# Optimization experiments

Hardware: AMD Instinct MI355X
Metric: run time of the kernel (lower is better)

## Reference

```python
import jax, jax.numpy as jnp
import numpy as np

H = 768   # hidden (cell) size
P = 256   # projection size
I = 80    # input feature dim
L = 3     # model_num_layers
B, T = 256, 400


def setup_inputs() -> dict:
    key = jax.random.key(0)
    ks = jax.random.split(key, 16)
    s = 0.05
    inp = {"x": jax.random.normal(ks[0], (B, T, I), dtype=jnp.float32)}
    in_dims = [I, P, P]
    for l in range(L):
        inp[f"Wx{l}"] = jax.random.normal(ks[1 + 4 * l], (in_dims[l], 4 * H), dtype=jnp.float32) * s
        inp[f"Wh{l}"] = jax.random.normal(ks[2 + 4 * l], (P, 4 * H), dtype=jnp.float32) * s
        inp[f"b{l}"] = jnp.zeros((4 * H,), dtype=jnp.float32)
        inp[f"Wp{l}"] = jax.random.normal(ks[3 + 4 * l], (H, P), dtype=jnp.float32) * s
    inp["W"] = jax.random.normal(ks[13], (P, P), dtype=jnp.float32) * s
    inp["lb"] = jnp.zeros((P,), dtype=jnp.float32)
    return inp


def _lstmp_layer(x, Wx, Wh, b, Wp, c0, h0):
    # Precompute input contribution to gates: [B, T, 4H]
    xg = jnp.einsum("bti,ig->btg", x, Wx) + b

    def step(carry, xg_t):
        c, h = carry
        gates = xg_t + h @ Wh              # [B, 4H]
        i, f, g, o = jnp.split(gates, 4, axis=-1)
        i = jax.nn.sigmoid(i)
        f = jax.nn.sigmoid(f)
        g = jnp.tanh(g)
        o = jax.nn.sigmoid(o)
        c = f * c + i * g                  # [B, H]
        h = (o * jnp.tanh(c)) @ Wp         # [B, P] projected hidden
        return (c, h), h

    (c, h), hs = jax.lax.scan(step, (c0, h0), jnp.swapaxes(xg, 0, 1))
    return jnp.swapaxes(hs, 0, 1), c, h   # seq_out [B,T,P], final c, h


def reference(x, Wx0, Wh0, b0, Wp0, Wx1, Wh1, b1, Wp1, Wx2, Wh2, b2, Wp2, W, lb):
    batch = x.shape[0]
    c = jnp.zeros((batch, H), dtype=x.dtype)
    h = jnp.zeros((batch, P), dtype=x.dtype)
    seq = x
    params = [(Wx0, Wh0, b0, Wp0), (Wx1, Wh1, b1, Wp1), (Wx2, Wh2, b2, Wp2)]
    for (Wx, Wh, b, Wp) in params:
        seq, c, h = _lstmp_layer(seq, Wx, Wh, b, Wp, c, h)
    embeds_raw = jax.nn.relu(seq.mean(axis=1) @ W.T + lb)   # [B, P]
    norm = jnp.linalg.norm(embeds_raw, axis=1, keepdims=True)
    return embeds_raw / norm
```

## Files before the change

kernel.cpp:

```cpp
#include <hip/hip_runtime.h>
#include <cstdint>
#include <cstddef>


typedef __attribute__((ext_vector_type(8))) short bf16x8;
typedef __attribute__((ext_vector_type(4))) float f32x4;
typedef __attribute__((ext_vector_type(2))) int i32x2;

#define TT 400
#define NB 256
#define IIP 96
#define HH 768
#define PP 256
#define G4 3072
#define WGJ 48
#define SMEMB (131072 + 2048)

__device__ __forceinline__ short f2bf(float f) {
  unsigned u = __builtin_bit_cast(unsigned, f);
  unsigned r = u + 0x7FFFu + ((u >> 16) & 1u);
  return (short)(r >> 16);
}
__device__ __forceinline__ float sigf(float x) { return 1.0f / (1.0f + __expf(-x)); }
__device__ __forceinline__ float tanh_(float x) { return 1.0f - 2.0f / (__expf(2.0f * x) + 1.0f); }

__device__ __forceinline__ void ld_co(bf16x8* d, const void* p) {
  asm volatile("global_load_dwordx4 %0, %1, off sc0 sc1" : "=v"(*d) : "v"(p));
}
__device__ __forceinline__ void st_co_b64(void* p, i32x2 v) {
  asm volatile("global_store_dwordx2 %0, %1, off sc0 sc1" :: "v"(p), "v"(v) : "memory");
}
__device__ __forceinline__ void st_co_b32(void* p, int v) {
  asm volatile("global_store_dword %0, %1, off sc0 sc1" :: "v"(p), "v"(v) : "memory");
}
#define WAIT_TIE24(u) \
  asm volatile("s_waitcnt vmcnt(0)" \
    : "+v"(u[0]),"+v"(u[1]),"+v"(u[2]),"+v"(u[3]),"+v"(u[4]),"+v"(u[5]), \
      "+v"(u[6]),"+v"(u[7]),"+v"(u[8]),"+v"(u[9]),"+v"(u[10]),"+v"(u[11]), \
      "+v"(u[12]),"+v"(u[13]),"+v"(u[14]),"+v"(u[15]),"+v"(u[16]),"+v"(u[17]), \
      "+v"(u[18]),"+v"(u[19]),"+v"(u[20]),"+v"(u[21]),"+v"(u[22]),"+v"(u[23]))


__global__ void k_xb(const float* __restrict__ x, short* __restrict__ xb) {
  int idx = blockIdx.x * 256 + threadIdx.x;
  if (idx >= TT * NB * 80) return;
  int i = idx % 80, tb = idx / 80;
  int b = tb % NB, t = tb / NB;
  xb[(size_t)(t * NB + b) * IIP + i] = f2bf(x[(size_t)(b * TT + t) * 80 + i]);
}

__global__ void k_makeB(const float* __restrict__ Wx, const float* __restrict__ Wp,
                        const float* __restrict__ Wh, short* __restrict__ out,
                        int K, int KIN, int INDIM) {
  int np = blockIdx.x * 256 + threadIdx.x;
  int k = blockIdx.y;
  int j2 = np >> 6, wj = np & 63, ntg = wj >> 4, cc = wj & 15;
  int col = ntg * HH + j2 * 16 + cc;
  float v;
  if (k < KIN) {
    v = (k < INDIM) ? Wx[(size_t)k * G4 + col] : 0.0f;
  } else {
    float a = 0.f;
    int kr = k - KIN;
    for (int q = 0; q < PP; ++q)
      a = fmaf(Wp[(size_t)kr * PP + q], Wh[(size_t)q * G4 + col], a);
    v = a;
  }
  out[(size_t)np * K + k] = f2bf(v);
}

__global__ void k_wpT(const float* __restrict__ Wp, short* __restrict__ WpT) {
  int idx = blockIdx.x * 256 + threadIdx.x;
  if (idx >= PP * HH) return;
  int n = idx % PP, k = idx / PP;
  WpT[(size_t)n * HH + k] = f2bf(Wp[(size_t)k * PP + n]);
}

__global__ void k_whT(const float* __restrict__ Wh, short* __restrict__ WhT) {
  int idx = blockIdx.x * 256 + threadIdx.x;
  if (idx >= G4 * PP) return;
  int np = idx % G4, k = idx / G4;
  int j2 = np >> 6, wj = np & 63, ntg = wj >> 4, cc = wj & 15;
  int col = ntg * HH + j2 * 16 + cc;
  WhT[(size_t)np * PP + k] = f2bf(Wh[(size_t)k * G4 + col]);
}

__global__ void k_pb(const float* b0, const float* b1, const float* b2, float* pb) {
  int n = blockIdx.x * 256 + threadIdx.x;
  if (n >= 3 * G4) return;
  int l = n / G4, np = n % G4;
  int j2 = np >> 6, wj = np & 63, ntg = wj >> 4, cc = wj & 15;
  int col = ntg * HH + j2 * 16 + cc;
  pb[n] = (l == 0 ? b0 : (l == 1 ? b1 : b2))[col];
}

__global__ void k_wt(const float* __restrict__ W, float* __restrict__ Wt) {
  int idx = blockIdx.x * 256 + threadIdx.x;
  int q = idx >> 8, p = idx & 255;
  Wt[idx] = W[p * 256 + q];
}


__device__ __forceinline__ void bar_arrive(int* slots, int j, int tid, int& arr) {
  asm volatile("s_waitcnt vmcnt(0)" ::: "memory");
  __syncthreads();
  ++arr;
  if (tid == 0) st_co_b32(slots + j * 4, arr);
}
__device__ __forceinline__ void bar_wait(const int* slots, int lane, int wv, int arr) {
  if (wv == 0) {
    const int* p = slots + (lane < 48 ? lane : 47) * 4;
    for (;;) {
      int v;
      asm volatile("global_load_dword %0, %1, off sc0 sc1\n\ts_waitcnt vmcnt(0)"
                   : "=v"(v) : "v"(p) : "memory");
      if (__all(v >= arr)) break;
      __builtin_amdgcn_s_sleep(1);
    }
  }
  __syncthreads();
}


template <int K>
__device__ __forceinline__ void stageB(const short* __restrict__ Bw, char* BsC, int j, int tid) {
  const char* src = (const char*)(Bw + (size_t)j * 64 * K);
  constexpr int UPR = K / 8;
  constexpr int ITERS = 64 * UPR / 256;
  #pragma unroll
  for (int it = 0; it < ITERS; ++it) {
    int u = it * 256 + tid;
    int wj = u / UPR;
    int k0 = (u - wj * UPR) * 8;
    bf16x8 v = *(const bf16x8*)(src + (size_t)wj * (K * 2) + k0 * 2);
    int gi = ((k0 >> 3) ^ (wj >> 1)) & 3;
    *(bf16x8*)(BsC + ((k0 >> 5) << 12) + (wj << 6) + (gi << 4)) = v;
  }
}


template <int CIN, bool DOPROJ, bool DOSUM>
__device__ __forceinline__ void layer_run(
    const char* BsC, short* UtS,
    const short* __restrict__ inS, const int inStr,
    const short* __restrict__ WpT, short* __restrict__ projOut,
    const float* __restrict__ pbL,
    short* __restrict__ U, int* slots,
    float* creg, float* sreg, f32x4* accInit,
    const int g, const int j, const int tid, int& arr)
{
  const int lane = tid & 63, wv = tid >> 6;
  const int c0 = lane & 15, rg = lane >> 4;
  const int row0 = g * 64;

  float bias[4];
  int fbB[4];
  #pragma unroll
  for (int nt = 0; nt < 4; ++nt) {
    bias[nt] = pbL[j * 64 + nt * 16 + c0];
    fbB[nt] = ((nt * 16 + c0) << 6) | (((rg ^ (c0 >> 1)) & 3) << 4);
  }
  const short* wb = DOPROJ ? (WpT + (size_t)(j * 16 + c0) * HH + rg * 8) : nullptr;

  for (int t = 0; t < TT; ++t) {
    const int pw = t & 1, pr = pw ^ 1;
    const short* aX = inS + (size_t)t * NB * inStr + (size_t)(row0 + wv * 16 + c0) * inStr + rg * 8;
    const short* aU = U + (size_t)pr * NB * HH + (size_t)(row0 + wv * 16 + c0) * HH + rg * 8;

    f32x4 zz = {0.f, 0.f, 0.f, 0.f};
    f32x4 acc[4];
    #pragma unroll
    for (int nt = 0; nt < 4; ++nt) acc[nt] = (t == 0) ? accInit[nt] : zz;

    bf16x8 xf[CIN];
    #pragma unroll
    for (int c = 0; c < CIN; ++c) xf[c] = *(const bf16x8*)(aX + c * 32);
    #pragma unroll
    for (int c = 0; c < CIN; ++c)
      #pragma unroll
      for (int nt = 0; nt < 4; ++nt)
        acc[nt] = __builtin_amdgcn_mfma_f32_16x16x32_bf16(
            xf[c], *(const bf16x8*)(BsC + (c << 12) + fbB[nt]), acc[nt], 0, 0, 0);

    if (t > 0) {
      bar_wait(slots, lane, wv, arr);
      bf16x8 uf[24];
      #pragma unroll
      for (int c = 0; c < 24; ++c) ld_co(&uf[c], aU + c * 32);
      WAIT_TIE24(uf);
      #pragma unroll
      for (int c = 0; c < 24; ++c)
        #pragma unroll
        for (int nt = 0; nt < 4; ++nt)
          acc[nt] = __builtin_amdgcn_mfma_f32_16x16x32_bf16(
              uf[c], *(const bf16x8*)(BsC + ((CIN + c) << 12) + fbB[nt]), acc[nt], 0, 0, 0);
      if (DOPROJ && j < 16) {
        f32x4 pacc = zz;
        #pragma unroll
        for (int c = 0; c < 24; ++c)
          pacc = __builtin_amdgcn_mfma_f32_16x16x32_bf16(
              uf[c], *(const bf16x8*)(wb + c * 32), pacc, 0, 0, 0);
        #pragma unroll
        for (int r = 0; r < 4; ++r)
          projOut[(size_t)(t - 1) * NB * PP + (size_t)(row0 + wv * 16 + rg * 4 + r) * PP + j * 16 + c0] = f2bf(pacc[r]);
      }
    }

    #pragma unroll
    for (int r = 0; r < 4; ++r) {
      float gi = acc[0][r] + bias[0];
      float gf = acc[1][r] + bias[1];
      float gg = acc[2][r] + bias[2];
      float go = acc[3][r] + bias[3];
      float cc2 = sigf(gf) * creg[r] + sigf(gi) * tanh_(gg);
      creg[r] = cc2;
      float uu = sigf(go) * tanh_(cc2);
      if (DOSUM) sreg[r] += uu;
      UtS[(wv * 16 + rg * 4 + r) * 16 + c0] = f2bf(uu);
    }
    __syncthreads();
    {
      int row = tid >> 2, q = tid & 3;
      i32x2 v = *(const i32x2*)(UtS + row * 16 + q * 4);
      st_co_b64((short*)U + (size_t)pw * NB * HH + (size_t)(row0 + row) * HH + j * 16 + q * 4, v);
    }
    bar_arrive(slots, j, tid, arr);
  }
}


__global__ void __launch_bounds__(256, 1) lstm_fused(
    const short* __restrict__ xb,
    const short* __restrict__ B0w, const short* __restrict__ B1w, const short* __restrict__ B2w,
    const float* __restrict__ pb,
    const short* __restrict__ WpT0, const short* __restrict__ WpT1,
    const short* __restrict__ WhT1, const short* __restrict__ WhT2,
    short* __restrict__ U, short* __restrict__ seqH,
    float* __restrict__ S, int* __restrict__ cnts)
{
  extern __shared__ char smem[];
  char* BsC = smem;
  short* UtS = (short*)(smem + 131072);
  const int bx = blockIdx.x;
  const int xcd = bx & 7;
  const int g = xcd >> 1;
  const int j = (xcd & 1) * 24 + (bx >> 3);
  const int tid = threadIdx.x;
  const int lane = tid & 63, wv = tid >> 6, c0 = lane & 15, rg = lane >> 4;
  const int row0 = g * 64;
  int* slots = cnts + g * 192;
  int arr = 0;
  float creg[4] = {0.f, 0.f, 0.f, 0.f}, sreg[4] = {0.f, 0.f, 0.f, 0.f};
  f32x4 zz = {0.f, 0.f, 0.f, 0.f};
  f32x4 accInit[4];
  #pragma unroll
  for (int nt = 0; nt < 4; ++nt) accInit[nt] = zz;

  stageB<864>(B0w, BsC, j, tid);
  __syncthreads();

  layer_run<3, true, false>(BsC, UtS, xb, IIP, WpT0, seqH, pb, U, slots,
                            creg, sreg, accInit, g, j, tid, arr);

  bar_wait(slots, lane, wv, arr);
  if (j < 16) {
    bf16x8 uf[24];
    const short* aU1 = U + (size_t)1 * NB * HH + (size_t)(row0 + wv * 16 + c0) * HH + rg * 8;
    #pragma unroll
    for (int c = 0; c < 24; ++c) ld_co(&uf[c], aU1 + c * 32);
    WAIT_TIE24(uf);
    const short* wb0 = WpT0 + (size_t)(j * 16 + c0) * HH + rg * 8;
    f32x4 pacc = zz;
    #pragma unroll
    for (int c = 0; c < 24; ++c)
      pacc = __builtin_amdgcn_mfma_f32_16x16x32_bf16(uf[c], *(const bf16x8*)(wb0 + c * 32), pacc, 0, 0, 0);
    #pragma unroll
    for (int r = 0; r < 4; ++r)
      seqH[(size_t)399 * NB * PP + (size_t)(row0 + wv * 16 + rg * 4 + r) * PP + j * 16 + c0] = f2bf(pacc[r]);
  }
  __threadfence();
  bar_arrive(slots, j, tid, arr);
  bar_wait(slots, lane, wv, arr);
  __threadfence();
  {
    const short* aseq = seqH + (size_t)399 * NB * PP + (size_t)(row0 + wv * 16 + c0) * PP + rg * 8;
    #pragma unroll
    for (int nt = 0; nt < 4; ++nt) accInit[nt] = zz;
    #pragma unroll
    for (int c = 0; c < 8; ++c) {
      bf16x8 a = *(const bf16x8*)(aseq + c * 32);
      #pragma unroll
      for (int nt = 0; nt < 4; ++nt) {
        bf16x8 b = *(const bf16x8*)(WhT1 + (size_t)(j * 64 + nt * 16 + c0) * PP + c * 32 + rg * 8);
        accInit[nt] = __builtin_amdgcn_mfma_f32_16x16x32_bf16(a, b, accInit[nt], 0, 0, 0);
      }
    }
  }
  __syncthreads();
  stageB<1024>(B1w, BsC, j, tid);
  __syncthreads();

  layer_run<8, true, false>(BsC, UtS, seqH, PP, WpT1, seqH, pb + G4, U, slots,
                            creg, sreg, accInit, g, j, tid, arr);

  bar_wait(slots, lane, wv, arr);
  if (j < 16) {
    bf16x8 uf[24];
    const short* aU1 = U + (size_t)1 * NB * HH + (size_t)(row0 + wv * 16 + c0) * HH + rg * 8;
    #pragma unroll
    for (int c = 0; c < 24; ++c) ld_co(&uf[c], aU1 + c * 32);
    WAIT_TIE24(uf);
    const short* wb1 = WpT1 + (size_t)(j * 16 + c0) * HH + rg * 8;
    f32x4 pacc = zz;
    #pragma unroll
    for (int c = 0; c < 24; ++c)
      pacc = __builtin_amdgcn_mfma_f32_16x16x32_bf16(uf[c], *(const bf16x8*)(wb1 + c * 32), pacc, 0, 0, 0);
    #pragma unroll
    for (int r = 0; r < 4; ++r)
      seqH[(size_t)399 * NB * PP + (size_t)(row0 + wv * 16 + rg * 4 + r) * PP + j * 16 + c0] = f2bf(pacc[r]);
  }
  __threadfence();
  bar_arrive(slots, j, tid, arr);
  bar_wait(slots, lane, wv, arr);
  __threadfence();
  {
    const short* aseq = seqH + (size_t)399 * NB * PP + (size_t)(row0 + wv * 16 + c0) * PP + rg * 8;
    #pragma unroll
    for (int nt = 0; nt < 4; ++nt) accInit[nt] = zz;
    #pragma unroll
    for (int c = 0; c < 8; ++c) {
      bf16x8 a = *(const bf16x8*)(aseq + c * 32);
      #pragma unroll
      for (int nt = 0; nt < 4; ++nt) {
        bf16x8 b = *(const bf16x8*)(WhT2 + (size_t)(j * 64 + nt * 16 + c0) * PP + c * 32 + rg * 8);
        accInit[nt] = __builtin_amdgcn_mfma_f32_16x16x32_bf16(a, b, accInit[nt], 0, 0, 0);
      }
    }
  }
  __syncthreads();
  stageB<1024>(B2w, BsC, j, tid);
  __syncthreads();

  layer_run<8, false, true>(BsC, UtS, seqH, PP, nullptr, nullptr, pb + 2 * G4, U, slots,
                            creg, sreg, accInit, g, j, tid, arr);

  #pragma unroll
  for (int r = 0; r < 4; ++r)
    S[(size_t)(row0 + wv * 16 + rg * 4 + r) * HH + j * 16 + c0] = sreg[r];
}


__global__ void k_mh(const float* __restrict__ S, const float* __restrict__ Wp2, float* __restrict__ mh) {
  __shared__ float sl[HH];
  int b = blockIdx.x, p = threadIdx.x;
  for (int i = p; i < HH; i += 256) sl[i] = S[(size_t)b * HH + i] * (1.0f / 400.0f);
  __syncthreads();
  float a = 0.f;
  for (int k = 0; k < HH; ++k) a = fmaf(sl[k], Wp2[(size_t)k * PP + p], a);
  mh[b * PP + p] = a;
}

__global__ void k_out(const float* __restrict__ mh, const float* __restrict__ Wt,
                      const float* __restrict__ lb, float* __restrict__ out) {
  __shared__ float ml[PP];
  __shared__ float red[PP];
  int b = blockIdx.x, p = threadIdx.x;
  ml[p] = mh[b * PP + p];
  __syncthreads();
  float z = lb[p];
  for (int q = 0; q < PP; ++q) z = fmaf(ml[q], Wt[q * PP + p], z);
  z = fmaxf(z, 0.0f);
  red[p] = z * z;
  __syncthreads();
  for (int st = 128; st > 0; st >>= 1) { if (p < st) red[p] += red[p + st]; __syncthreads(); }
  out[b * PP + p] = z / sqrtf(red[0]);
}


extern "C" void kernel_launch(void* const* d_in, const int* in_sizes, int n_in,
                              void* d_out, int out_size, void* d_ws, size_t ws_size,
                              hipStream_t stream) {
  (void)in_sizes; (void)n_in; (void)out_size; (void)ws_size;
  const float* x   = (const float*)d_in[0];
  const float* Wx0 = (const float*)d_in[1];
  const float* Wh0 = (const float*)d_in[2];
  const float* b0  = (const float*)d_in[3];
  const float* Wp0 = (const float*)d_in[4];
  const float* Wx1 = (const float*)d_in[5];
  const float* Wh1 = (const float*)d_in[6];
  const float* b1  = (const float*)d_in[7];
  const float* Wp1 = (const float*)d_in[8];
  const float* Wx2 = (const float*)d_in[9];
  const float* Wh2 = (const float*)d_in[10];
  const float* b2  = (const float*)d_in[11];
  const float* Wp2 = (const float*)d_in[12];
  const float* W   = (const float*)d_in[13];
  const float* lb  = (const float*)d_in[14];

  char* w = (char*)d_ws;
  auto take = [&](size_t bytes) { char* p = w; w += (bytes + 255) & ~(size_t)255; return p; };
  short* xb    = (short*)take((size_t)TT * NB * IIP * 2);
  short* B0w   = (short*)take((size_t)G4 * 864 * 2);
  short* B1w   = (short*)take((size_t)G4 * 1024 * 2);
  short* B2w   = (short*)take((size_t)G4 * 1024 * 2);
  float* pbw   = (float*)take((size_t)3 * G4 * 4);
  short* WpT0  = (short*)take((size_t)PP * HH * 2);
  short* WpT1  = (short*)take((size_t)PP * HH * 2);
  short* WhT1  = (short*)take((size_t)G4 * PP * 2);
  short* WhT2  = (short*)take((size_t)G4 * PP * 2);
  short* U     = (short*)take((size_t)2 * NB * HH * 2);
  short* seqH  = (short*)take((size_t)TT * NB * PP * 2);
  float* Sw    = (float*)take((size_t)NB * HH * 4);
  float* mhw   = (float*)take((size_t)NB * PP * 4);
  float* Wtw   = (float*)take((size_t)PP * PP * 4);
  int*   cnts  = (int*)take(4 * 192 * 4);

  hipMemsetAsync(xb, 0, (size_t)TT * NB * IIP * 2, stream);
  hipMemsetAsync(cnts, 0, 4 * 192 * 4, stream);

  k_xb<<<(TT * NB * 80 + 255) / 256, 256, 0, stream>>>(x, xb);
  k_makeB<<<dim3(12, 864), 256, 0, stream>>>(Wx0, Wp0, Wh0, B0w, 864, 96, 80);
  k_makeB<<<dim3(12, 1024), 256, 0, stream>>>(Wx1, Wp1, Wh1, B1w, 1024, 256, 256);
  k_makeB<<<dim3(12, 1024), 256, 0, stream>>>(Wx2, Wp2, Wh2, B2w, 1024, 256, 256);
  k_wpT<<<(PP * HH + 255) / 256, 256, 0, stream>>>(Wp0, WpT0);
  k_wpT<<<(PP * HH + 255) / 256, 256, 0, stream>>>(Wp1, WpT1);
  k_whT<<<(G4 * PP + 255) / 256, 256, 0, stream>>>(Wh1, WhT1);
  k_whT<<<(G4 * PP + 255) / 256, 256, 0, stream>>>(Wh2, WhT2);
  k_pb<<<(3 * G4 + 255) / 256, 256, 0, stream>>>(b0, b1, b2, pbw);
  k_wt<<<(PP * PP) / 256, 256, 0, stream>>>(W, Wtw);

  hipFuncSetAttribute((const void*)lstm_fused,
                      hipFuncAttributeMaxDynamicSharedMemorySize, SMEMB);
  lstm_fused<<<4 * WGJ, 256, SMEMB, stream>>>(xb, B0w, B1w, B2w, pbw, WpT0, WpT1,
                                              WhT1, WhT2, U, seqH, Sw, cnts);

  k_mh<<<NB, 256, 0, stream>>>(Sw, Wp2, mhw);
  k_out<<<NB, 256, 0, stream>>>(mhw, Wtw, lb, (float*)d_out);
}
```

Before: 11.95 ms.

## Split fused persistent LSTM into per-layer kernels with atomic-counter barriers

Replaces the single persistent kernel covering all three layers with one launch per layer, plus a small kernel that computes the initial hidden-to-gate term between layers. The per-workgroup flag-slot barrier becomes a single atomic counter per batch group that waits on a target count. The 24-load coherent asm block with its tied waitcnt becomes plain loads, and the projection MFMA is moved after the barrier arrive so it overlaps with other workgroups' progress. Projection stores now go through LDS and are written as coalesced 64-bit stores. This adds kernel launch overhead and a global round trip for the cell state and initial gates, and the plain (non-sc) loads of U may read stale cached data after the acquire fence.

```diff
diff --git a/kernel.cpp b/kernel.cpp
--- a/kernel.cpp
+++ b/kernel.cpp
@@ -24,21 +24,15 @@
 __device__ __forceinline__ float sigf(float x) { return 1.0f / (1.0f + __expf(-x)); }
 __device__ __forceinline__ float tanh_(float x) { return 1.0f - 2.0f / (__expf(2.0f * x) + 1.0f); }
 
-__device__ __forceinline__ void ld_co(bf16x8* d, const void* p) {
-  asm volatile("global_load_dwordx4 %0, %1, off sc0 sc1" : "=v"(*d) : "v"(p));
-}
 __device__ __forceinline__ void st_co_b64(void* p, i32x2 v) {
   asm volatile("global_store_dwordx2 %0, %1, off sc0 sc1" :: "v"(p), "v"(v) : "memory");
 }
-__device__ __forceinline__ void st_co_b32(void* p, int v) {
-  asm volatile("global_store_dword %0, %1, off sc0 sc1" :: "v"(p), "v"(v) : "memory");
-}
-#define WAIT_TIE24(u) \
-  asm volatile("s_waitcnt vmcnt(0)" \
-    : "+v"(u[0]),"+v"(u[1]),"+v"(u[2]),"+v"(u[3]),"+v"(u[4]),"+v"(u[5]), \
-      "+v"(u[6]),"+v"(u[7]),"+v"(u[8]),"+v"(u[9]),"+v"(u[10]),"+v"(u[11]), \
-      "+v"(u[12]),"+v"(u[13]),"+v"(u[14]),"+v"(u[15]),"+v"(u[16]),"+v"(u[17]), \
-      "+v"(u[18]),"+v"(u[19]),"+v"(u[20]),"+v"(u[21]),"+v"(u[22]),"+v"(u[23]))
+__device__ __forceinline__ int ld_flag(const int* p) {
+  int v;
+  asm volatile("global_load_dword %0, %1, off sc0 sc1\n\ts_waitcnt vmcnt(0)"
+               : "=v"(v) : "v"(p) : "memory");
+  return v;
+}
 
 
 __global__ void k_xb(const float* __restrict__ x, short* __restrict__ xb) {
@@ -100,23 +94,50 @@
   Wt[idx] = W[p * 256 + q];
 }
 
-
-__device__ __forceinline__ void bar_arrive(int* slots, int j, int tid, int& arr) {
+__global__ void __launch_bounds__(256) k_trans2(
+    const short* __restrict__ seqF,
+    const short* __restrict__ WhT, float* __restrict__ xg0b)
+{
+  const int blk = blockIdx.x;
+  const int g = blk & 3, j = blk >> 2;
+  const int tid = threadIdx.x, lane = tid & 63, wv = tid >> 6;
+  const int c0 = lane & 15, rg = lane >> 4;
+  const int row0 = g * 64;
+  const short* aseq = seqF + (size_t)(row0 + wv * 16 + c0) * PP + rg * 8;
+
+  f32x4 zz = {0.f, 0.f, 0.f, 0.f};
+  f32x4 acc[4];
+  #pragma unroll
+  for (int nt = 0; nt < 4; ++nt) acc[nt] = zz;
+  #pragma unroll
+  for (int c = 0; c < 8; ++c) {
+    bf16x8 a = *(const bf16x8*)(aseq + c * 32);
+    #pragma unroll
+    for (int nt = 0; nt < 4; ++nt) {
+      bf16x8 b = *(const bf16x8*)(WhT + (size_t)(j * 64 + nt * 16 + c0) * PP + c * 32 + rg * 8);
+      acc[nt] = __builtin_amdgcn_mfma_f32_16x16x32_bf16(a, b, acc[nt], 0, 0, 0);
+    }
+  }
+  #pragma unroll
+  for (int nt = 0; nt < 4; ++nt)
+    #pragma unroll
+    for (int r = 0; r < 4; ++r)
+      xg0b[(size_t)(row0 + wv * 16 + rg * 4 + r) * G4 + j * 64 + nt * 16 + c0] = acc[nt][r];
+}
+
+
+__device__ __forceinline__ void bar_arrive(int* cnt, int tid) {
   asm volatile("s_waitcnt vmcnt(0)" ::: "memory");
   __syncthreads();
-  ++arr;
-  if (tid == 0) st_co_b32(slots + j * 4, arr);
-}
-__device__ __forceinline__ void bar_wait(const int* slots, int lane, int wv, int arr) {
+  if (tid == 0) {
+    int old = __hip_atomic_fetch_add(cnt, 1, __ATOMIC_RELAXED, __HIP_MEMORY_SCOPE_AGENT);
+    (void)old;
+  }
+}
+__device__ __forceinline__ void bar_wait(const int* cnt, int wv, int target) {
   if (wv == 0) {
-    const int* p = slots + (lane < 48 ? lane : 47) * 4;
-    for (;;) {
-      int v;
-      asm volatile("global_load_dword %0, %1, off sc0 sc1\n\ts_waitcnt vmcnt(0)"
-                   : "=v"(v) : "v"(p) : "memory");
-      if (__all(v >= arr)) break;
-      __builtin_amdgcn_s_sleep(1);
-    }
+    while (ld_flag(cnt) < target) __builtin_amdgcn_s_sleep(2);
+    __builtin_amdgcn_fence(__ATOMIC_ACQUIRE, "agent");
   }
   __syncthreads();
 }
@@ -139,104 +160,14 @@
 }
 
 
-template <int CIN, bool DOPROJ, bool DOSUM>
-__device__ __forceinline__ void layer_run(
-    const char* BsC, short* UtS,
+template <int CIN, int DOPROJ, int DOSUM, int USEXG>
+__global__ void __launch_bounds__(256, 1) k_layer(
+    const short* __restrict__ Bw,
     const short* __restrict__ inS, const int inStr,
     const short* __restrict__ WpT, short* __restrict__ projOut,
     const float* __restrict__ pbL,
-    short* __restrict__ U, int* slots,
-    float* creg, float* sreg, f32x4* accInit,
-    const int g, const int j, const int tid, int& arr)
-{
-  const int lane = tid & 63, wv = tid >> 6;
-  const int c0 = lane & 15, rg = lane >> 4;
-  const int row0 = g * 64;
-
-  float bias[4];
-  int fbB[4];
-  #pragma unroll
-  for (int nt = 0; nt < 4; ++nt) {
-    bias[nt] = pbL[j * 64 + nt * 16 + c0];
-    fbB[nt] = ((nt * 16 + c0) << 6) | (((rg ^ (c0 >> 1)) & 3) << 4);
-  }
-  const short* wb = DOPROJ ? (WpT + (size_t)(j * 16 + c0) * HH + rg * 8) : nullptr;
-
-  for (int t = 0; t < TT; ++t) {
-    const int pw = t & 1, pr = pw ^ 1;
-    const short* aX = inS + (size_t)t * NB * inStr + (size_t)(row0 + wv * 16 + c0) * inStr + rg * 8;
-    const short* aU = U + (size_t)pr * NB * HH + (size_t)(row0 + wv * 16 + c0) * HH + rg * 8;
-
-    f32x4 zz = {0.f, 0.f, 0.f, 0.f};
-    f32x4 acc[4];
-    #pragma unroll
-    for (int nt = 0; nt < 4; ++nt) acc[nt] = (t == 0) ? accInit[nt] : zz;
-
-    bf16x8 xf[CIN];
-    #pragma unroll
-    for (int c = 0; c < CIN; ++c) xf[c] = *(const bf16x8*)(aX + c * 32);
-    #pragma unroll
-    for (int c = 0; c < CIN; ++c)
-      #pragma unroll
-      for (int nt = 0; nt < 4; ++nt)
-        acc[nt] = __builtin_amdgcn_mfma_f32_16x16x32_bf16(
-            xf[c], *(const bf16x8*)(BsC + (c << 12) + fbB[nt]), acc[nt], 0, 0, 0);
-
-    if (t > 0) {
-      bar_wait(slots, lane, wv, arr);
-      bf16x8 uf[24];
-      #pragma unroll
-      for (int c = 0; c < 24; ++c) ld_co(&uf[c], aU + c * 32);
-      WAIT_TIE24(uf);
-      #pragma unroll
-      for (int c = 0; c < 24; ++c)
-        #pragma unroll
-        for (int nt = 0; nt < 4; ++nt)
-          acc[nt] = __builtin_amdgcn_mfma_f32_16x16x32_bf16(
-              uf[c], *(const bf16x8*)(BsC + ((CIN + c) << 12) + fbB[nt]), acc[nt], 0, 0, 0);
-      if (DOPROJ && j < 16) {
-        f32x4 pacc = zz;
-        #pragma unroll
-        for (int c = 0; c < 24; ++c)
-          pacc = __builtin_amdgcn_mfma_f32_16x16x32_bf16(
-              uf[c], *(const bf16x8*)(wb + c * 32), pacc, 0, 0, 0);
-        #pragma unroll
-        for (int r = 0; r < 4; ++r)
-          projOut[(size_t)(t - 1) * NB * PP + (size_t)(row0 + wv * 16 + rg * 4 + r) * PP + j * 16 + c0] = f2bf(pacc[r]);
-      }
-    }
-
-    #pragma unroll
-    for (int r = 0; r < 4; ++r) {
-      float gi = acc[0][r] + bias[0];
-      float gf = acc[1][r] + bias[1];
-      float gg = acc[2][r] + bias[2];
-      float go = acc[3][r] + bias[3];
-      float cc2 = sigf(gf) * creg[r] + sigf(gi) * tanh_(gg);
-      creg[r] = cc2;
-      float uu = sigf(go) * tanh_(cc2);
-      if (DOSUM) sreg[r] += uu;
-      UtS[(wv * 16 + rg * 4 + r) * 16 + c0] = f2bf(uu);
-    }
-    __syncthreads();
-    {
-      int row = tid >> 2, q = tid & 3;
-      i32x2 v = *(const i32x2*)(UtS + row * 16 + q * 4);
-      st_co_b64((short*)U + (size_t)pw * NB * HH + (size_t)(row0 + row) * HH + j * 16 + q * 4, v);
-    }
-    bar_arrive(slots, j, tid, arr);
-  }
-}
-
-
-__global__ void __launch_bounds__(256, 1) lstm_fused(
-    const short* __restrict__ xb,
-    const short* __restrict__ B0w, const short* __restrict__ B1w, const short* __restrict__ B2w,
-    const float* __restrict__ pb,
-    const short* __restrict__ WpT0, const short* __restrict__ WpT1,
-    const short* __restrict__ WhT1, const short* __restrict__ WhT2,
-    short* __restrict__ U, short* __restrict__ seqH,
-    float* __restrict__ S, int* __restrict__ cnts)
+    short* __restrict__ U, float* __restrict__ Cw, float* __restrict__ S,
+    const float* __restrict__ xg0b, int* __restrict__ cntBase)
 {
   extern __shared__ char smem[];
   char* BsC = smem;
@@ -248,105 +179,128 @@
   const int tid = threadIdx.x;
   const int lane = tid & 63, wv = tid >> 6, c0 = lane & 15, rg = lane >> 4;
   const int row0 = g * 64;
-  int* slots = cnts + g * 192;
-  int arr = 0;
-  float creg[4] = {0.f, 0.f, 0.f, 0.f}, sreg[4] = {0.f, 0.f, 0.f, 0.f};
+  int* cnt = (int*)((char*)cntBase + g * 4096);
+  constexpr int K = CIN * 32 + 768;
+
+  stageB<K>(Bw, BsC, j, tid);
+
+  float creg[4], sreg[4] = {0.f, 0.f, 0.f, 0.f};
+  #pragma unroll
+  for (int r = 0; r < 4; ++r)
+    creg[r] = USEXG ? Cw[(size_t)(row0 + wv * 16 + rg * 4 + r) * HH + j * 16 + c0] : 0.f;
+
+  float bias[4];
+  int fbB[4];
+  #pragma unroll
+  for (int nt = 0; nt < 4; ++nt) {
+    bias[nt] = pbL[j * 64 + nt * 16 + c0];
+    fbB[nt] = ((nt * 16 + c0) << 6) | (((rg ^ (c0 >> 1)) & 3) << 4);
+  }
+  const short* wb = DOPROJ ? (WpT + (size_t)(j * 16 + c0) * HH + rg * 8) : nullptr;
   f32x4 zz = {0.f, 0.f, 0.f, 0.f};
-  f32x4 accInit[4];
-  #pragma unroll
-  for (int nt = 0; nt < 4; ++nt) accInit[nt] = zz;
-
-  stageB<864>(B0w, BsC, j, tid);
-  __syncthreads();
-
-  layer_run<3, true, false>(BsC, UtS, xb, IIP, WpT0, seqH, pb, U, slots,
-                            creg, sreg, accInit, g, j, tid, arr);
-
-  bar_wait(slots, lane, wv, arr);
-  if (j < 16) {
+
+  __syncthreads();
+
+  for (int t = 0; t < TT; ++t) {
+    const int pw = t & 1, pr = pw ^ 1;
+    const short* aX = inS + (size_t)t * NB * inStr + (size_t)(row0 + wv * 16 + c0) * inStr + rg * 8;
+    const short* aU = U + (size_t)pr * NB * HH + (size_t)(row0 + wv * 16 + c0) * HH + rg * 8;
+
+    f32x4 acc[4];
+    if (USEXG && t == 0) {
+      #pragma unroll
+      for (int nt = 0; nt < 4; ++nt)
+        #pragma unroll
+        for (int r = 0; r < 4; ++r)
+          acc[nt][r] = xg0b[(size_t)(row0 + wv * 16 + rg * 4 + r) * G4 + j * 64 + nt * 16 + c0];
+    } else {
+      #pragma unroll
+      for (int nt = 0; nt < 4; ++nt) acc[nt] = zz;
+    }
+
+    bf16x8 xf[CIN];
+    #pragma unroll
+    for (int c = 0; c < CIN; ++c) xf[c] = *(const bf16x8*)(aX + c * 32);
+    #pragma unroll
+    for (int c = 0; c < CIN; ++c)
+      #pragma unroll
+      for (int nt = 0; nt < 4; ++nt)
+        acc[nt] = __builtin_amdgcn_mfma_f32_16x16x32_bf16(
+            xf[c], *(const bf16x8*)(BsC + (c << 12) + fbB[nt]), acc[nt], 0, 0, 0);
+
     bf16x8 uf[24];
+    if (t > 0) {
+      bar_wait(cnt, wv, WGJ * t);
+      #pragma unroll
+      for (int c = 0; c < 24; ++c) uf[c] = *(const bf16x8*)(aU + c * 32);
+      #pragma unroll
+      for (int c = 0; c < 24; ++c)
+        #pragma unroll
+        for (int nt = 0; nt < 4; ++nt)
+          acc[nt] = __builtin_amdgcn_mfma_f32_16x16x32_bf16(
+              uf[c], *(const bf16x8*)(BsC + ((CIN + c) << 12) + fbB[nt]), acc[nt], 0, 0, 0);
+    }
+
+    #pragma unroll
+    for (int r = 0; r < 4; ++r) {
+      float gi = acc[0][r] + bias[0];
+      float gf = acc[1][r] + bias[1];
+      float gg = acc[2][r] + bias[2];
+      float go = acc[3][r] + bias[3];
+      float cc2 = sigf(gf) * creg[r] + sigf(gi) * tanh_(gg);
+      creg[r] = cc2;
+      float uu = sigf(go) * tanh_(cc2);
+      if (DOSUM) sreg[r] += uu;
+      UtS[(wv * 16 + rg * 4 + r) * 16 + c0] = f2bf(uu);
+    }
+    __syncthreads();
+    {
+      int row = tid >> 2, q = tid & 3;
+      i32x2 v = *(const i32x2*)(UtS + row * 16 + q * 4);
+      st_co_b64((short*)U + (size_t)pw * NB * HH + (size_t)(row0 + row) * HH + j * 16 + q * 4, v);
+    }
+    bar_arrive(cnt, tid);
+
+    if (DOPROJ && j < 16 && t > 0) {
+      f32x4 pacc = zz;
+      #pragma unroll
+      for (int c = 0; c < 24; ++c)
+        pacc = __builtin_amdgcn_mfma_f32_16x16x32_bf16(
+            uf[c], *(const bf16x8*)(wb + c * 32), pacc, 0, 0, 0);
+      #pragma unroll
+      for (int r = 0; r < 4; ++r)
+        UtS[(wv * 16 + rg * 4 + r) * 16 + c0] = f2bf(pacc[r]);
+      __syncthreads();
+      int row = tid >> 2, q = tid & 3;
+      i32x2 v = *(const i32x2*)(UtS + row * 16 + q * 4);
+      st_co_b64(projOut + (size_t)(t - 1) * NB * PP + (size_t)(row0 + row) * PP + j * 16 + q * 4, v);
+    }
+  }
+
+  bar_wait(cnt, wv, WGJ * TT);
+  if (DOPROJ && j < 16) {
     const short* aU1 = U + (size_t)1 * NB * HH + (size_t)(row0 + wv * 16 + c0) * HH + rg * 8;
-    #pragma unroll
-    for (int c = 0; c < 24; ++c) ld_co(&uf[c], aU1 + c * 32);
-    WAIT_TIE24(uf);
-    const short* wb0 = WpT0 + (size_t)(j * 16 + c0) * HH + rg * 8;
     f32x4 pacc = zz;
     #pragma unroll
-    for (int c = 0; c < 24; ++c)
-      pacc = __builtin_amdgcn_mfma_f32_16x16x32_bf16(uf[c], *(const bf16x8*)(wb0 + c * 32), pacc, 0, 0, 0);
+    for (int c = 0; c < 24; ++c) {
+      bf16x8 a = *(const bf16x8*)(aU1 + c * 32);
+      pacc = __builtin_amdgcn_mfma_f32_16x16x32_bf16(a, *(const bf16x8*)(wb + c * 32), pacc, 0, 0, 0);
+    }
     #pragma unroll
     for (int r = 0; r < 4; ++r)
-      seqH[(size_t)399 * NB * PP + (size_t)(row0 + wv * 16 + rg * 4 + r) * PP + j * 16 + c0] = f2bf(pacc[r]);
-  }
-  __threadfence();
-  bar_arrive(slots, j, tid, arr);
-  bar_wait(slots, lane, wv, arr);
-  __threadfence();
-  {
-    const short* aseq = seqH + (size_t)399 * NB * PP + (size_t)(row0 + wv * 16 + c0) * PP + rg * 8;
-    #pragma unroll
-    for (int nt = 0; nt < 4; ++nt) accInit[nt] = zz;
-    #pragma unroll
-    for (int c = 0; c < 8; ++c) {
-      bf16x8 a = *(const bf16x8*)(aseq + c * 32);
-      #pragma unroll
-      for (int nt = 0; nt < 4; ++nt) {
-        bf16x8 b = *(const bf16x8*)(WhT1 + (size_t)(j * 64 + nt * 16 + c0) * PP + c * 32 + rg * 8);
-        accInit[nt] = __builtin_amdgcn_mfma_f32_16x16x32_bf16(a, b, accInit[nt], 0, 0, 0);
-      }
-    }
-  }
-  __syncthreads();
-  stageB<1024>(B1w, BsC, j, tid);
-  __syncthreads();
-
-  layer_run<8, true, false>(BsC, UtS, seqH, PP, WpT1, seqH, pb + G4, U, slots,
-                            creg, sreg, accInit, g, j, tid, arr);
-
-  bar_wait(slots, lane, wv, arr);
-  if (j < 16) {
-    bf16x8 uf[24];
-    const short* aU1 = U + (size_t)1 * NB * HH + (size_t)(row0 + wv * 16 + c0) * HH + rg * 8;
-    #pragma unroll
-    for (int c = 0; c < 24; ++c) ld_co(&uf[c], aU1 + c * 32);
-    WAIT_TIE24(uf);
-    const short* wb1 = WpT1 + (size_t)(j * 16 + c0) * HH + rg * 8;
-    f32x4 pacc = zz;
-    #pragma unroll
-    for (int c = 0; c < 24; ++c)
-      pacc = __builtin_amdgcn_mfma_f32_16x16x32_bf16(uf[c], *(const bf16x8*)(wb1 + c * 32), pacc, 0, 0, 0);
-    #pragma unroll
-    for (int r = 0; r < 4; ++r)
-      seqH[(size_t)399 * NB * PP + (size_t)(row0 + wv * 16 + rg * 4 + r) * PP + j * 16 + c0] = f2bf(pacc[r]);
-  }
-  __threadfence();
-  bar_arrive(slots, j, tid, arr);
-  bar_wait(slots, lane, wv, arr);
-  __threadfence();
-  {
-    const short* aseq = seqH + (size_t)399 * NB * PP + (size_t)(row0 + wv * 16 + c0) * PP + rg * 8;
-    #pragma unroll
-    for (int nt = 0; nt < 4; ++nt) accInit[nt] = zz;
-    #pragma unroll
-    for (int c = 0; c < 8; ++c) {
-      bf16x8 a = *(const bf16x8*)(aseq + c * 32);
-      #pragma unroll
-      for (int nt = 0; nt < 4; ++nt) {
-        bf16x8 b = *(const bf16x8*)(WhT2 + (size_t)(j * 64 + nt * 16 + c0) * PP + c * 32 + rg * 8);
-        accInit[nt] = __builtin_amdgcn_mfma_f32_16x16x32_bf16(a, b, accInit[nt], 0, 0, 0);
-      }
-    }
-  }
-  __syncthreads();
-  stageB<1024>(B2w, BsC, j, tid);
-  __syncthreads();
-
-  layer_run<8, false, true>(BsC, UtS, seqH, PP, nullptr, nullptr, pb + 2 * G4, U, slots,
-                            creg, sreg, accInit, g, j, tid, arr);
-
-  #pragma unroll
-  for (int r = 0; r < 4; ++r)
-    S[(size_t)(row0 + wv * 16 + rg * 4 + r) * HH + j * 16 + c0] = sreg[r];
+      UtS[(wv * 16 + rg * 4 + r) * 16 + c0] = f2bf(pacc[r]);
+    __syncthreads();
+    int row = tid >> 2, q = tid & 3;
+    i32x2 v = *(const i32x2*)(UtS + row * 16 + q * 4);
+    st_co_b64(projOut + (size_t)399 * NB * PP + (size_t)(row0 + row) * PP + j * 16 + q * 4, v);
+  }
+
+  #pragma unroll
+  for (int r = 0; r < 4; ++r) {
+    size_t idx = (size_t)(row0 + wv * 16 + rg * 4 + r) * HH + j * 16 + c0;
+    Cw[idx] = creg[r];
+    if (DOSUM) S[idx] = sreg[r];
+  }
 }
 
 
@@ -398,7 +352,7 @@
   const float* lb  = (const float*)d_in[14];
 
   char* w = (char*)d_ws;
-  auto take = [&](size_t bytes) { char* p = w; w += (bytes + 255) & ~(size_t)255; return p; };
+  auto take = [&](size_t bytes) { char* p = w; w += (bytes + 4095) & ~(size_t)4095; return p; };
   short* xb    = (short*)take((size_t)TT * NB * IIP * 2);
   short* B0w   = (short*)take((size_t)G4 * 864 * 2);
   short* B1w   = (short*)take((size_t)G4 * 1024 * 2);
@@ -410,13 +364,15 @@
   short* WhT2  = (short*)take((size_t)G4 * PP * 2);
   short* U     = (short*)take((size_t)2 * NB * HH * 2);
   short* seqH  = (short*)take((size_t)TT * NB * PP * 2);
+  float* xg0b  = (float*)take((size_t)NB * G4 * 4);
+  float* Cw    = (float*)take((size_t)NB * HH * 4);
   float* Sw    = (float*)take((size_t)NB * HH * 4);
   float* mhw   = (float*)take((size_t)NB * PP * 4);
   float* Wtw   = (float*)take((size_t)PP * PP * 4);
-  int*   cnts  = (int*)take(4 * 192 * 4);
+  int*   cnts  = (int*)take(3 * 4 * 4096);
 
   hipMemsetAsync(xb, 0, (size_t)TT * NB * IIP * 2, stream);
-  hipMemsetAsync(cnts, 0, 4 * 192 * 4, stream);
+  hipMemsetAsync(cnts, 0, 3 * 4 * 4096, stream);
 
   k_xb<<<(TT * NB * 80 + 255) / 256, 256, 0, stream>>>(x, xb);
   k_makeB<<<dim3(12, 864), 256, 0, stream>>>(Wx0, Wp0, Wh0, B0w, 864, 96, 80);
@@ -429,10 +385,26 @@
   k_pb<<<(3 * G4 + 255) / 256, 256, 0, stream>>>(b0, b1, b2, pbw);
   k_wt<<<(PP * PP) / 256, 256, 0, stream>>>(W, Wtw);
 
-  hipFuncSetAttribute((const void*)lstm_fused,
+  hipFuncSetAttribute((const void*)k_layer<3, 1, 0, 0>,
                       hipFuncAttributeMaxDynamicSharedMemorySize, SMEMB);
-  lstm_fused<<<4 * WGJ, 256, SMEMB, stream>>>(xb, B0w, B1w, B2w, pbw, WpT0, WpT1,
-                                              WhT1, WhT2, U, seqH, Sw, cnts);
+  hipFuncSetAttribute((const void*)k_layer<8, 1, 0, 1>,
+                      hipFuncAttributeMaxDynamicSharedMemorySize, SMEMB);
+  hipFuncSetAttribute((const void*)k_layer<8, 0, 1, 1>,
+                      hipFuncAttributeMaxDynamicSharedMemorySize, SMEMB);
+
+  k_layer<3, 1, 0, 0><<<4 * WGJ, 256, SMEMB, stream>>>(
+      B0w, xb, IIP, WpT0, seqH, pbw + 0 * G4, U, Cw, Sw, xg0b,
+      (int*)((char*)cnts + 0 * 16384));
+  k_trans2<<<4 * WGJ, 256, 0, stream>>>(seqH + (size_t)399 * NB * PP, WhT1, xg0b);
+
+  k_layer<8, 1, 0, 1><<<4 * WGJ, 256, SMEMB, stream>>>(
+      B1w, seqH, PP, WpT1, seqH, pbw + 1 * G4, U, Cw, Sw, xg0b,
+      (int*)((char*)cnts + 1 * 16384));
+  k_trans2<<<4 * WGJ, 256, 0, stream>>>(seqH + (size_t)399 * NB * PP, WhT2, xg0b);
+
+  k_layer<8, 0, 1, 1><<<4 * WGJ, 256, SMEMB, stream>>>(
+      B2w, seqH, PP, nullptr, nullptr, pbw + 2 * G4, U, Cw, Sw, xg0b,
+      (int*)((char*)cnts + 2 * 16384));
 
   k_mh<<<NB, 256, 0, stream>>>(Sw, Wp2, mhw);
   k_out<<<NB, 256, 0, stream>>>(mhw, Wtw, lb, (float*)d_out);
```

Result: faster. 11.29 ms (-5.5%).
